# Kernel tuning notes

Hardware: AMD Instinct MI355X
Metric: run time of the kernel (lower is better)

## Reference

```python
import jax, jax.numpy as jnp
import numpy as np

B, S, E, H = 4, 1024, 1024, 16
HD = E // H
EPS = 1e-10


def setup_inputs() -> dict:
    key = jax.random.key(0)
    ks = jax.random.split(key, 10)
    w = lambda k: jax.random.normal(k, (E, E), jnp.float32) * 0.02
    b = lambda k: jax.random.normal(k, (E,), jnp.float32) * 0.02
    return {
        "query": jax.random.normal(ks[0], (B, S, E), jnp.float32),
        "Wq": w(ks[1]), "bq": b(ks[2]),
        "Wk": w(ks[3]), "bk": b(ks[4]),
        "Wv": w(ks[5]), "bv": b(ks[6]),
        "Wo": w(ks[7]), "bo": b(ks[8]),
        "alpha": jnp.array(1.0, jnp.float32),
    }


def reference(query, Wq, bq, Wk, bk, Wv, bv, Wo, bo, alpha):
    scale = 1.0 / np.sqrt(HD)
    # projections -> [B, H, S, HD]
    def heads(x, W, bias):
        return (x @ W.T + bias).reshape(B, S, H, HD).transpose(0, 2, 1, 3)
    Q = heads(query, Wq, bq)
    K = heads(query, Wk, bk)
    V = heads(query, Wv, bv)
    # raw scores [B, H, S, S]
    scores = jnp.einsum('bhqd,bhkd->bhqk', Q, K) * scale
    # 2D FFT over the (q, k) plane
    scores_fft = jnp.fft.fft2(scores, axes=(-2, -1))
    # spectral filter: exp(i * alpha * arctan(log|F| + eps))
    phase = alpha * jnp.arctan(jnp.log(jnp.abs(scores_fft) + EPS))
    filt = jnp.exp(1j * phase)
    scores_filtered = jnp.fft.ifft2(scores_fft * filt, axes=(-2, -1)).real
    # softmax over keys (dropout is identity at eval)
    attn = jax.nn.softmax(scores_filtered, axis=-1)
    ctx = jnp.einsum('bhqk,bhkd->bhqd', attn, V)
    ctx = ctx.transpose(0, 2, 1, 3).reshape(B, S, E)
    return ctx @ Wo.T + bo
```

## Files before the change

kernel.cpp:

```cpp
#include <hip/hip_runtime.h>
#include <hip/hip_fp16.h>


typedef __attribute__((ext_vector_type(8))) short short8;
typedef __attribute__((ext_vector_type(8))) _Float16 half8;
typedef __attribute__((ext_vector_type(4))) float f32x4;

#define PITCH 40
#define PITCH1 72

__device__ __forceinline__ float bf2f(short v) {
  return __uint_as_float(((unsigned)(unsigned short)v) << 16);
}
__device__ __forceinline__ short f2bf(float f) {
  unsigned u = __float_as_uint(f);
  u += 0x7FFFu + ((u >> 16) & 1u);
  return (short)(u >> 16);
}

__device__ __forceinline__ short8 ld8(const void* p, size_t idx, int isf32) {
  short8 r;
  if (isf32) {
    const float* f = (const float*)p + idx;
    float4 a = *(const float4*)f;
    float4 b = *(const float4*)(f + 4);
    r[0] = f2bf(a.x); r[1] = f2bf(a.y); r[2] = f2bf(a.z); r[3] = f2bf(a.w);
    r[4] = f2bf(b.x); r[5] = f2bf(b.y); r[6] = f2bf(b.z); r[7] = f2bf(b.w);
  } else {
    r = *(const short8*)((const short*)p + idx);
  }
  return r;
}
__device__ __forceinline__ float ldf(const void* p, int idx, int isf32) {
  return isf32 ? ((const float*)p)[idx] : bf2f(((const short*)p)[idx]);
}

__device__ __forceinline__ float2 cmul(float2 a, float2 b) {
  return make_float2(a.x * b.x - a.y * b.y, a.x * b.y + a.y * b.x);
}
__device__ __forceinline__ float2 cmulc(float2 a, float2 b) {
  return make_float2(a.x * b.x + a.y * b.y, a.y * b.x - a.x * b.y);
}
__device__ __forceinline__ float2 cadd(float2 a, float2 b) {
  return make_float2(a.x + b.x, a.y + b.y);
}
__device__ __forceinline__ float2 csub(float2 a, float2 b) {
  return make_float2(a.x - b.x, a.y - b.y);
}


template <int SGN>
__device__ __forceinline__ void dft16_dif(float2* x) {
  const float C16[8] = {1.f, 0.92387953f, 0.70710678f, 0.38268343f,
                        0.f, -0.38268343f, -0.70710678f, -0.92387953f};
  const float S16[8] = {0.f, 0.38268343f, 0.70710678f, 0.92387953f,
                        1.f, 0.92387953f, 0.70710678f, 0.38268343f};
#pragma unroll
  for (int h = 8; h >= 1; h >>= 1)
#pragma unroll
    for (int b = 0; b < 16; b += 2 * h)
#pragma unroll
      for (int i = 0; i < h; ++i) {
        const int e = i * (8 / h);
        float2 u = x[b + i], v = x[b + i + h];
        x[b + i] = cadd(u, v);
        float2 d = csub(u, v);
        float2 w = make_float2(C16[e], SGN > 0 ? S16[e] : -S16[e]);
        x[b + i + h] = (e == 0) ? d : cmul(d, w);
      }
}

__device__ __forceinline__ void dit16_inv(float2* x) {
  const float C16[8] = {1.f, 0.92387953f, 0.70710678f, 0.38268343f,
                        0.f, -0.38268343f, -0.70710678f, -0.92387953f};
  const float S16[8] = {0.f, 0.38268343f, 0.70710678f, 0.92387953f,
                        1.f, 0.92387953f, 0.70710678f, 0.38268343f};
#pragma unroll
  for (int h = 1; h <= 8; h <<= 1)
#pragma unroll
    for (int b = 0; b < 16; b += 2 * h)
#pragma unroll
      for (int i = 0; i < h; ++i) {
        const int e = i * (8 / h);
        float2 w = make_float2(C16[e], -S16[e]);
        float2 u = x[b + i];
        float2 vh = (e == 0) ? x[b + i + h] : cmulc(x[b + i + h], w);
        x[b + i] = cadd(u, vh);
        x[b + i + h] = csub(u, vh);
      }
}

template <int SGN>
__device__ __forceinline__ void midtw(float2* x, int lane) {
  const int rho[16] = {0, 8, 4, 12, 2, 10, 6, 14, 1, 9, 5, 13, 3, 11, 7, 15};
  float s, c;
  __sincosf((float)lane * 0.00613592315f, &s, &c);
  float2 w = make_float2(c, SGN > 0 ? s : -s);
  float2 run = w;
  x[8] = cmul(x[8], run);
#pragma unroll
  for (int e = 2; e < 16; ++e) {
    run = cmul(run, w);
    x[rho[e]] = cmul(x[rho[e]], run);
  }
}

template <int SGN>
__device__ __forceinline__ void xlane_dif(float2* x, int lane) {
#pragma unroll
  for (int h = 32; h >= 1; h >>= 1) {
    const int e = (lane & (h - 1)) * (32 / h);
    float s, c;
    __sincosf((float)e * 0.09817477042f, &s, &c);
    float2 w = make_float2(c, SGN > 0 ? s : -s);
    const bool hi = (lane & h) != 0;
#pragma unroll
    for (int r = 0; r < 16; ++r) {
      float2 t = x[r];
      float2 p;
      p.x = __shfl_xor(t.x, h, 64);
      p.y = __shfl_xor(t.y, h, 64);
      x[r] = hi ? cmul(csub(p, t), w) : cadd(t, p);
    }
  }
}

template <int SGN>
__device__ __forceinline__ void wfft1024_dif(float2* x, int lane) {
  dft16_dif<SGN>(x);
  midtw<SGN>(x, lane);
  xlane_dif<SGN>(x, lane);
}

template <int SGN>
__device__ __forceinline__ void midtw2(float2* x, float2* y, int lane) {
  const int rho[16] = {0, 8, 4, 12, 2, 10, 6, 14, 1, 9, 5, 13, 3, 11, 7, 15};
  float s, c;
  __sincosf((float)lane * 0.00613592315f, &s, &c);
  float2 w = make_float2(c, SGN > 0 ? s : -s);
  float2 run = w;
  x[8] = cmul(x[8], run);
  y[8] = cmul(y[8], run);
#pragma unroll
  for (int e = 2; e < 16; ++e) {
    run = cmul(run, w);
    x[rho[e]] = cmul(x[rho[e]], run);
    y[rho[e]] = cmul(y[rho[e]], run);
  }
}

__device__ __forceinline__ void midtw_inv2(float2* x, float2* y, int lane) {
  const int rho[16] = {0, 8, 4, 12, 2, 10, 6, 14, 1, 9, 5, 13, 3, 11, 7, 15};
  float s, c;
  __sincosf((float)lane * 0.00613592315f, &s, &c);
  float2 w = make_float2(c, -s);
  float2 run = w;
  x[8] = cmulc(x[8], run);
  y[8] = cmulc(y[8], run);
#pragma unroll
  for (int e = 2; e < 16; ++e) {
    run = cmul(run, w);
    x[rho[e]] = cmulc(x[rho[e]], run);
    y[rho[e]] = cmulc(y[rho[e]], run);
  }
}

template <int SGN>
__device__ __forceinline__ void xlane_dif2(float2* x, float2* y, int lane) {
#pragma unroll
  for (int h = 32; h >= 1; h >>= 1) {
    const int e = (lane & (h - 1)) * (32 / h);
    float s, c;
    __sincosf((float)e * 0.09817477042f, &s, &c);
    float2 w = make_float2(c, SGN > 0 ? s : -s);
    const bool hi = (lane & h) != 0;
#pragma unroll
    for (int r = 0; r < 16; ++r) {
      float2 t = x[r];
      float2 p;
      p.x = __shfl_xor(t.x, h, 64);
      p.y = __shfl_xor(t.y, h, 64);
      x[r] = hi ? cmul(csub(p, t), w) : cadd(t, p);
    }
#pragma unroll
    for (int r = 0; r < 16; ++r) {
      float2 t = y[r];
      float2 p;
      p.x = __shfl_xor(t.x, h, 64);
      p.y = __shfl_xor(t.y, h, 64);
      y[r] = hi ? cmul(csub(p, t), w) : cadd(t, p);
    }
  }
}

__device__ __forceinline__ void xlane_dit_inv2(float2* x, float2* y, int lane) {
#pragma unroll
  for (int h = 1; h <= 32; h <<= 1) {
    const int e = (lane & (h - 1)) * (32 / h);
    float s, c;
    __sincosf((float)e * 0.09817477042f, &s, &c);
    float2 w = make_float2(c, -s);
    const bool hi = (lane & h) != 0;
#pragma unroll
    for (int r = 0; r < 16; ++r) {
      float2 t = x[r];
      if (hi) t = cmulc(t, w);
      float2 p;
      p.x = __shfl_xor(t.x, h, 64);
      p.y = __shfl_xor(t.y, h, 64);
      x[r] = hi ? csub(p, t) : cadd(t, p);
    }
#pragma unroll
    for (int r = 0; r < 16; ++r) {
      float2 t = y[r];
      if (hi) t = cmulc(t, w);
      float2 p;
      p.x = __shfl_xor(t.x, h, 64);
      p.y = __shfl_xor(t.y, h, 64);
      y[r] = hi ? csub(p, t) : cadd(t, p);
    }
  }
}

template <int SGN>
__device__ __forceinline__ void wfft1024_dif2(float2* x, float2* y, int lane) {
  dft16_dif<SGN>(x);
  dft16_dif<SGN>(y);
  midtw2<SGN>(x, y, lane);
  xlane_dif2<SGN>(x, y, lane);
}
__device__ __forceinline__ void wfft1024_inv2(float2* x, float2* y, int lane) {
  xlane_dit_inv2(x, y, lane);
  midtw_inv2(x, y, lane);
  dit16_inv(x);
  dit16_inv(y);
}

__device__ __forceinline__ float gainw(float re, float im, float alpha, bool a1) {
  float mag2 = re * re + im * im;
  float t = 0.5f * __logf(mag2 + 1e-20f);
  if (a1) return __builtin_amdgcn_rsqf(fmaf(t, t, 1.0f)) * (1.0f / 1048576.0f);
  return __cosf(alpha * atanf(t)) * (1.0f / 1048576.0f);
}

__global__ void k0_detect(const unsigned* __restrict__ q,
                          const void* __restrict__ alphap, int* __restrict__ flags) {
  __shared__ float smax[256];
  __shared__ int szero[256];
  int t = threadIdx.x;
  float mx = 0.f; int zc = 0;
  for (int i = t; i < 16384; i += 256) {
    unsigned w = q[i];
    unsigned lo = w & 0xFFFFu;
    float v = fabsf(__uint_as_float(lo << 16));
    if (!(v <= 1e30f)) v = 1e30f;
    mx = fmaxf(mx, v);
    zc += (lo == 0u);
  }
  smax[t] = mx; szero[t] = zc;
  __syncthreads();
  for (int s = 128; s > 0; s >>= 1) {
    if (t < s) { smax[t] = fmaxf(smax[t], smax[t + s]); szero[t] += szero[t + s]; }
    __syncthreads();
  }
  if (t == 0) {
    int isf32 = (smax[0] > 100.f) || (szero[0] > 12288);
    flags[0] = isf32;
    float alpha = isf32 ? *(const float*)alphap : bf2f(*(const short*)alphap);
    ((float*)flags)[1] = alpha;
  }
}

__global__ __launch_bounds__(256) void k1_qkv(
    const void* __restrict__ x,
    const void* __restrict__ Wq, const void* __restrict__ bq,
    const void* __restrict__ Wk, const void* __restrict__ bk,
    const void* __restrict__ Wv, const void* __restrict__ bv,
    short* __restrict__ Qt, short* __restrict__ Kt, short* __restrict__ Vt,
    const int* __restrict__ flags)
{
  __shared__ __align__(16) char smem[128 * PITCH1 * 2 * 2];
  short* As = (short*)smem;
  short* Bs = As + 128 * PITCH1;
  short* Ct = (short*)smem;
  const int isf32 = flags[0];
  const int t = threadIdx.x;
  const int lb = blockIdx.x;
  const int m0 = ((lb & 7) * 4 + ((lb >> 3) & 3)) * 128;
  const int n0 = (lb >> 5) * 128;
  const int which = blockIdx.y;
  const void* __restrict__ W = (which == 0) ? Wq : (which == 1) ? Wk : Wv;
  const void* __restrict__ bias = (which == 0) ? bq : (which == 1) ? bk : bv;
  const int lane = t & 63, wvi = t >> 6;
  const int wr = wvi >> 1, wc = wvi & 1;
  const int lm = lane & 15, lq = lane >> 4;
  f32x4 acc[4][4] = {};

  for (int k0 = 0; k0 < 1024; k0 += 64) {
    __syncthreads();
#pragma unroll
    for (int i = 0; i < 4; ++i) {
      int l = t + i * 256;
      int row = l >> 3, kk = (l & 7) << 3;
      *(short8*)&As[row * PITCH1 + kk] = ld8(x, (size_t)(m0 + row) * 1024 + k0 + kk, isf32);
      *(short8*)&Bs[row * PITCH1 + kk] = ld8(W, (size_t)(n0 + row) * 1024 + k0 + kk, isf32);
    }
    __syncthreads();
#pragma unroll
    for (int kh = 0; kh < 2; ++kh) {
      short8 af[4], bf[4];
#pragma unroll
      for (int a = 0; a < 4; ++a)
        af[a] = *(const short8*)&As[(wr * 64 + a * 16 + lm) * PITCH1 + kh * 32 + lq * 8];
#pragma unroll
      for (int b = 0; b < 4; ++b)
        bf[b] = *(const short8*)&Bs[(wc * 64 + b * 16 + lm) * PITCH1 + kh * 32 + lq * 8];
#pragma unroll
      for (int a = 0; a < 4; ++a)
#pragma unroll
        for (int b = 0; b < 4; ++b)
          acc[a][b] = __builtin_amdgcn_mfma_f32_16x16x32_bf16(af[a], bf[b], acc[a][b], 0, 0, 0);
    }
  }

  __syncthreads();
#pragma unroll
  for (int a = 0; a < 4; ++a)
#pragma unroll
    for (int b = 0; b < 4; ++b) {
      int col = wc * 64 + b * 16 + lm;
      float bv_ = ldf(bias, n0 + col, isf32);
#pragma unroll
      for (int r = 0; r < 4; ++r) {
        int row = wr * 64 + a * 16 + lq * 4 + r;
        Ct[row * 136 + col] = f2bf(acc[a][b][r] + bv_);
      }
    }
  __syncthreads();

  short* __restrict__ O = (which == 0) ? Qt : (which == 1) ? Kt : Vt;
#pragma unroll
  for (int j = 0; j < 8; ++j) {
    int id = t + j * 256;
    int d128 = id & 127, sg = (id >> 7) * 8;
    short vals[8];
#pragma unroll
    for (int i = 0; i < 8; ++i) vals[i] = Ct[(sg + i) * 136 + d128];
    int col = n0 + d128;
    int h = col >> 6, d = col & 63;
    int bb = m0 >> 10, sbase = (m0 & 1023) + sg;
    *(short8*)&O[(((size_t)(bb * 16 + h)) << 16) + ((size_t)d << 10) + sbase] = *(short8*)vals;
  }
}

__global__ __launch_bounds__(128) void kA_qkfft(
    const short* __restrict__ Qt, const short* __restrict__ Kt,
    __half2* __restrict__ Qhat, __half2* __restrict__ Khat)
{
  __shared__ float2 sbuf[2][1024];
  const int lane = threadIdx.x & 63, w = threadIdx.x >> 6;
  const int z = blockIdx.y;
  const int bx = blockIdx.x;
  if (bx < 16) {
    const short* qp = Qt + ((size_t)z << 16);
    const int d0 = bx * 4 + w * 2;
    float2 x[16], y[16];
#pragma unroll
    for (int j = 0; j < 16; ++j) {
      x[j] = make_float2(0.125f * bf2f(qp[(d0 << 10) + lane + 64 * j]), 0.f);
      y[j] = make_float2(0.125f * bf2f(qp[((d0 + 1) << 10) + lane + 64 * j]), 0.f);
    }
    wfft1024_dif2<-1>(x, y, lane);
    __half2* o0 = Qhat + (((size_t)(z * 64 + d0)) << 10);
    __half2* o1 = o0 + 1024;
#pragma unroll
    for (int r = 0; r < 16; ++r) {
      o0[lane + 64 * r] = __float22half2_rn(x[r]);
      o1[lane + 64 * r] = __float22half2_rn(y[r]);
    }
  } else {
    const short* kp = Kt + ((size_t)z << 16);
    const int p = (bx - 16) * 2 + w;
    const int d0 = 2 * p;
    float2 x[16];
#pragma unroll
    for (int j = 0; j < 16; ++j)
      x[j] = make_float2(bf2f(kp[(d0 << 10) + lane + 64 * j]),
                         bf2f(kp[((d0 + 1) << 10) + lane + 64 * j]));
    wfft1024_dif<-1>(x, lane);
    const int rho[16] = {0, 8, 4, 12, 2, 10, 6, 14, 1, 9, 5, 13, 3, 11, 7, 15};
    const int bl6 = ((lane & 1) << 5) | ((lane & 2) << 3) | ((lane & 4) << 1) |
                    ((lane & 8) >> 1) | ((lane & 16) >> 3) | ((lane & 32) >> 5);
    float2* buf = sbuf[w];
#pragma unroll
    for (int r = 0; r < 16; ++r) buf[rho[r] + 16 * bl6] = x[r];
    __half2* o0 = Khat + (size_t)(z * 64 + d0) * 520;
    __half2* o1 = o0 + 520;
#pragma unroll 1
    for (int jj = 0; jj < 9; ++jj) {
      int v = lane + 64 * jj;
      if (v <= 512) {
        float2 A = buf[v], B = buf[(1024 - v) & 1023];
        o0[v] = __float22half2_rn(make_float2((A.x + B.x) * 0.5f, (A.y - B.y) * 0.5f));
        o1[v] = __float22half2_rn(make_float2((A.y + B.y) * 0.5f, (B.x - A.x) * 0.5f));
      }
    }
  }
}

__global__ __launch_bounds__(256) void kB_specmm(
    const __half2* __restrict__ Qhat, const __half2* __restrict__ Khat,
    __half2* __restrict__ Ct, const int* __restrict__ flags, int bh0)
{
  __shared__ unsigned short Are[64][72], Aim[64][72], Bre[128][72], Bim[128][72];
  const int t = threadIdx.x;
  const int u0 = blockIdx.x * 128;
  const int v0 = blockIdx.y * 64;
  const int zl = blockIdx.z;
  const int z = bh0 + zl;
  const float alpha = ((const float*)flags)[1];
  const bool a1 = (alpha == 1.0f);
  {
    const int d = t >> 2;
    const ushort2* src = (const ushort2*)(Khat + (size_t)(z * 64 + d) * 520);
    int vb = (t & 3) * 16;
#pragma unroll
    for (int j = 0; j < 16; ++j) {
      int v = v0 + vb + j;
      if (v > 519) v = 519;
      ushort2 e = src[v];
      int row = vb + j;
      int dc = d ^ (((row >> 4) & 3) << 4);
      Are[row][dc] = e.x;
      Aim[row][dc] = e.y;
    }
    const ushort2* srcb = (const ushort2*)(Qhat + (((size_t)(z * 64 + d)) << 10) + u0);
    int ub = (t & 3) * 32;
#pragma unroll
    for (int j = 0; j < 32; ++j) {
      ushort2 e = srcb[ub + j];
      int row = ub + j;
      int dc = d ^ (((row >> 5) & 3) << 4);
      Bre[row][dc] = e.x;
      Bim[row][dc] = e.y;
    }
  }
  __syncthreads();

  const int lane = t & 63, wc = t >> 6;
  const int lm = lane & 15, lq = lane >> 4;
  f32x4 cre[4][2] = {}, cim[4][2] = {};
#pragma unroll
  for (int ks = 0; ks < 2; ++ks) {
    half8 ar[4], ai[4], aiN[4], br[2], bi[2];
#pragma unroll
    for (int a = 0; a < 4; ++a) {
      int dc = (ks * 32 + lq * 8) ^ ((a & 3) << 4);
      ar[a] = *(const half8*)&Are[a * 16 + lm][dc];
      ai[a] = *(const half8*)&Aim[a * 16 + lm][dc];
      int4 tm = *(int4*)&ai[a];
      tm.x ^= 0x80008000; tm.y ^= 0x80008000; tm.z ^= 0x80008000; tm.w ^= 0x80008000;
      aiN[a] = *(half8*)&tm;
    }
#pragma unroll
    for (int n = 0; n < 2; ++n) {
      int dc = (ks * 32 + lq * 8) ^ ((wc & 3) << 4);
      br[n] = *(const half8*)&Bre[wc * 32 + n * 16 + lm][dc];
      bi[n] = *(const half8*)&Bim[wc * 32 + n * 16 + lm][dc];
    }
#pragma unroll
    for (int a = 0; a < 4; ++a)
#pragma unroll
      for (int n = 0; n < 2; ++n) {
        cre[a][n] = __builtin_amdgcn_mfma_f32_16x16x32_f16(ar[a], br[n], cre[a][n], 0, 0, 0);
        cre[a][n] = __builtin_amdgcn_mfma_f32_16x16x32_f16(aiN[a], bi[n], cre[a][n], 0, 0, 0);
        cim[a][n] = __builtin_amdgcn_mfma_f32_16x16x32_f16(ar[a], bi[n], cim[a][n], 0, 0, 0);
        cim[a][n] = __builtin_amdgcn_mfma_f32_16x16x32_f16(ai[a], br[n], cim[a][n], 0, 0, 0);
      }
  }

  __half2* outp = Ct + (size_t)zl * 513 * 1024 + u0 + wc * 32;
#pragma unroll
  for (int a = 0; a < 4; ++a)
#pragma unroll
    for (int r = 0; r < 4; ++r) {
      int v = v0 + a * 16 + lq * 4 + r;
      if (v < 513) {
#pragma unroll
        for (int n = 0; n < 2; ++n) {
          float re = cre[a][n][r], im = cim[a][n][r];
          float wf = gainw(re, im, alpha, a1);
          outp[(size_t)v * 1024 + n * 16 + lm] =
              __float22half2_rn(make_float2(re * wf, im * wf));
        }
      }
    }
}

__global__ __launch_bounds__(256) void k4_invfft(__half2* __restrict__ Ct)
{
  const int lane = threadIdx.x & 63;
  const int w = threadIdx.x >> 6;
  const int gv0 = blockIdx.x * 8 + w * 2;
  if (gv0 > 512) return;
  const bool has1 = (gv0 + 1 <= 512);
  __half2* __restrict__ row0 = Ct + (size_t)blockIdx.y * 513 * 1024 + ((size_t)gv0 << 10);
  __half2* __restrict__ row1 = row0 + 1024;
  float2 x[16], y[16];
#pragma unroll
  for (int j = 0; j < 16; ++j) x[j] = __half22float2(row0[lane + 64 * j]);
  if (has1) {
#pragma unroll
    for (int j = 0; j < 16; ++j) y[j] = __half22float2(row1[lane + 64 * j]);
  } else {
#pragma unroll
    for (int j = 0; j < 16; ++j) y[j] = make_float2(0.f, 0.f);
  }
  wfft1024_inv2(x, y, lane);
#pragma unroll
  for (int j = 0; j < 16; ++j) row0[lane + 64 * j] = __float22half2_rn(x[j]);
  if (has1) {
#pragma unroll
    for (int j = 0; j < 16; ++j) row1[lane + 64 * j] = __float22half2_rn(y[j]);
  }
}

__global__ __launch_bounds__(512) void k56_softmax_av(
    const __half2* __restrict__ Ct, const short* __restrict__ Vt,
    short* __restrict__ ctx, int bh0)
{
  __shared__ __align__(16) char GP[33280];
  const int tid = threadIdx.x;
  const int q0 = blockIdx.x * 16, z = blockIdx.y;
  const int lane = tid & 63, w = tid >> 6;
  const int lm = lane & 15, lq = lane >> 4;
  const __half2* __restrict__ in = Ct + (size_t)z * 513 * 1024;
#define GROW(m) ((__half2*)(GP + 448 + (m) * 2052))
  for (int id = tid; id < 2052; id += 512) {
    int v = id >> 2, qq = (id & 3) * 4;
    int4 o = *(const int4*)&in[(size_t)v * 1024 + q0 + qq];
    __half2* op = (__half2*)&o;
#pragma unroll
    for (int i = 0; i < 4; ++i) GROW(qq + i)[v] = op[i];
  }
  short* P = (short*)GP;
  const int bl6 = ((lane & 1) << 5) | ((lane & 2) << 3) | ((lane & 4) << 1) |
                  ((lane & 8) >> 1) | ((lane & 16) >> 3) | ((lane & 32) >> 5);
  __syncthreads();

  const int p = w;
  const __half2* g1 = GROW(2 * p);
  const __half2* g2 = GROW(2 * p + 1);
  float2 x[16];
#pragma unroll
  for (int j = 0; j < 16; ++j) {
    int v = lane + 64 * j;
    float2 a, b;
    if (v <= 512) {
      a = __half22float2(g1[v]);
      b = __half22float2(g2[v]);
    } else {
      int v2 = 1024 - v;
      float2 aa = __half22float2(g1[v2]), bb = __half22float2(g2[v2]);
      a = make_float2(aa.x, -aa.y);
      b = make_float2(bb.x, -bb.y);
    }
    x[j] = make_float2(a.x - b.y, a.y + b.x);
  }

  wfft1024_dif<1>(x, lane);

  float m1 = -3.4e38f, m2 = -3.4e38f;
#pragma unroll
  for (int j = 0; j < 16; ++j) { m1 = fmaxf(m1, x[j].x); m2 = fmaxf(m2, x[j].y); }
#pragma unroll
  for (int s = 32; s > 0; s >>= 1) {
    m1 = fmaxf(m1, __shfl_xor(m1, s, 64));
    m2 = fmaxf(m2, __shfl_xor(m2, s, 64));
  }
  float s1 = 0.f, s2 = 0.f;
#pragma unroll
  for (int j = 0; j < 16; ++j) {
    float e1 = __expf(x[j].x - m1), e2 = __expf(x[j].y - m2);
    x[j] = make_float2(e1, e2);
    s1 += e1; s2 += e2;
  }
#pragma unroll
  for (int s = 32; s > 0; s >>= 1) {
    s1 += __shfl_xor(s1, s, 64);
    s2 += __shfl_xor(s2, s, 64);
  }
  float inv1 = 1.0f / s1, inv2 = 1.0f / s2;

  __syncthreads();

  {
    const int rho[16] = {0, 8, 4, 12, 2, 10, 6, 14, 1, 9, 5, 13, 3, 11, 7, 15};
#pragma unroll
    for (int j = 0; j < 16; ++j) {
      int k = rho[j] + 16 * bl6;
      P[(2 * p) * 1040 + k]     = f2bf(x[j].x * inv1);
      P[(2 * p + 1) * 1040 + k] = f2bf(x[j].y * inv2);
    }
  }
  __syncthreads();

  const short* __restrict__ Vp = Vt + ((size_t)(bh0 + z) << 16);
  f32x4 acc[4] = {};
#pragma unroll
  for (int ks = 0; ks < 4; ++ks) {
    int k0 = w * 128 + ks * 32;
    short8 a0 = *(const short8*)&P[lm * 1040 + k0 + lq * 8];
#pragma unroll
    for (int b = 0; b < 4; ++b) {
      short8 bv = *(const short8*)&Vp[(size_t)(b * 16 + lm) * 1024 + k0 + lq * 8];
      acc[b] = __builtin_amdgcn_mfma_f32_16x16x32_bf16(a0, bv, acc[b], 0, 0, 0);
    }
  }
  __syncthreads();
  float* red = (float*)GP;
#pragma unroll
  for (int b = 0; b < 4; ++b)
#pragma unroll
    for (int r = 0; r < 4; ++r)
      red[(w * 16 + lq * 4 + r) * 64 + b * 16 + lm] = acc[b][r];
  __syncthreads();
  if (tid < 256) {
    int q = tid >> 4, d0 = (tid & 15) * 4;
    float s0 = 0.f, s1_ = 0.f, s2_ = 0.f, s3 = 0.f;
#pragma unroll
    for (int ww = 0; ww < 8; ++ww) {
      const float* rr = &red[(ww * 16 + q) * 64 + d0];
      s0 += rr[0]; s1_ += rr[1]; s2_ += rr[2]; s3 += rr[3];
    }
    short o4[4] = {f2bf(s0), f2bf(s1_), f2bf(s2_), f2bf(s3)};
    *(int2*)&ctx[(((size_t)(bh0 + z)) << 16) + (size_t)(q0 + q) * 64 + d0] = *(int2*)o4;
  }
#undef GROW
}

__global__ __launch_bounds__(256) void k7_out(
    const short* __restrict__ ctx, const void* __restrict__ Wo,
    const void* __restrict__ bo, void* __restrict__ out,
    const int* __restrict__ flags)
{
  __shared__ __align__(16) char smem[128 * 136 * 2];
  short* As = (short*)smem;
  short* Bs = As + 128 * PITCH;
  short* Ct = (short*)smem;
  const int isf32 = flags[0];
  const int t = threadIdx.x;
  const int lb = blockIdx.x;
  const int m0 = ((lb & 7) * 4 + ((lb >> 3) & 3)) * 128;
  const int n0 = (lb >> 5) * 128;
  const int lane = t & 63, wvi = t >> 6;
  const int wr = wvi >> 1, wc = wvi & 1;
  const int lm = lane & 15, lq = lane >> 4;
  f32x4 acc[4][4] = {};

  for (int k0 = 0; k0 < 1024; k0 += 32) {
    __syncthreads();
#pragma unroll
    for (int i = 0; i < 2; ++i) {
      int l = t + i * 256;
      int row = l >> 2, kk = (l & 3) << 3;
      int n = m0 + row, e = k0 + kk;
      size_t aaddr = (((size_t)((n >> 10) * 16 + (e >> 6))) << 16) + (size_t)((n & 1023) << 6) + (e & 63);
      *(int4*)&As[row * PITCH + kk] = *(const int4*)&ctx[aaddr];
      *(short8*)&Bs[row * PITCH + kk] = ld8(Wo, (size_t)(n0 + row) * 1024 + e, isf32);
    }
    __syncthreads();
    short8 af[4], bf[4];
#pragma unroll
    for (int a = 0; a < 4; ++a) af[a] = *(const short8*)&As[(wr * 64 + a * 16 + lm) * PITCH + lq * 8];
#pragma unroll
    for (int b = 0; b < 4; ++b) bf[b] = *(const short8*)&Bs[(wc * 64 + b * 16 + lm) * PITCH + lq * 8];
#pragma unroll
    for (int a = 0; a < 4; ++a)
#pragma unroll
      for (int b = 0; b < 4; ++b)
        acc[a][b] = __builtin_amdgcn_mfma_f32_16x16x32_bf16(af[a], bf[b], acc[a][b], 0, 0, 0);
  }

  if (isf32) {
#pragma unroll
    for (int a = 0; a < 4; ++a)
#pragma unroll
      for (int b = 0; b < 4; ++b) {
        int col = n0 + wc * 64 + b * 16 + lm;
        float bo_ = ldf(bo, col, 1);
#pragma unroll
        for (int r = 0; r < 4; ++r) {
          int row = m0 + wr * 64 + a * 16 + lq * 4 + r;
          ((float*)out)[(size_t)row * 1024 + col] = acc[a][b][r] + bo_;
        }
      }
    return;
  }
  __syncthreads();
#pragma unroll
  for (int a = 0; a < 4; ++a)
#pragma unroll
    for (int b = 0; b < 4; ++b) {
      int col = wc * 64 + b * 16 + lm;
      float bo_ = ldf(bo, n0 + col, 0);
#pragma unroll
      for (int r = 0; r < 4; ++r) {
        int row = wr * 64 + a * 16 + lq * 4 + r;
        Ct[row * 136 + col] = f2bf(acc[a][b][r] + bo_);
      }
    }
  __syncthreads();
#pragma unroll
  for (int j = 0; j < 8; ++j) {
    int id = t + j * 256;
    int row = id >> 4, c16 = (id & 15) * 8;
    short8 v = *(const short8*)&Ct[row * 136 + c16];
    *(short8*)&((short*)out)[(size_t)(m0 + row) * 1024 + n0 + c16] = v;
  }
}

extern "C" void kernel_launch(void* const* d_in, const int* in_sizes, int n_in,
                              void* d_out, int out_size, void* d_ws, size_t ws_size,
                              hipStream_t stream)
{
  const void* x  = d_in[0];
  const void* Wq = d_in[1];
  const void* bq = d_in[2];
  const void* Wk = d_in[3];
  const void* bk = d_in[4];
  const void* Wv = d_in[5];
  const void* bv = d_in[6];
  const void* Wo = d_in[7];
  const void* bo = d_in[8];
  const void* alphap = d_in[9];
  char* ws = (char*)d_ws;

  const size_t PLANE_CT = (size_t)513 * 1024 * 4;
  const size_t QH_SZ = (size_t)64 * 64 * 1024 * 4;
  const size_t KH_SZ = (size_t)64 * 64 * 520 * 4;

  const size_t B_CT  = 0;
  const size_t B_VT  = 64 * PLANE_CT;
  const size_t B_CX  = B_VT + ((size_t)8u << 20);
  const size_t B_QH  = B_CX + ((size_t)8u << 20);
  const size_t B_KH  = B_QH + QH_SZ;
  const size_t B_FL  = B_KH + KH_SZ;
  const size_t B_NEED = B_FL + 256;

  if (ws_size >= B_NEED) {
    short*   Qt   = (short*)(ws);
    short*   Kt   = (short*)(ws + ((size_t)8u << 20));
    short*   Vt   = (short*)(ws + B_VT);
    short*   ctx  = (short*)(ws + B_CX);
    __half2* Ct   = (__half2*)(ws + B_CT);
    __half2* Qhat = (__half2*)(ws + B_QH);
    __half2* Khat = (__half2*)(ws + B_KH);
    int*     flags = (int*)(ws + B_FL);

    k0_detect<<<1, 256, 0, stream>>>((const unsigned*)x, alphap, flags);
    k1_qkv<<<dim3(256, 3), 256, 0, stream>>>(x, Wq, bq, Wk, bk, Wv, bv, Qt, Kt, Vt, flags);
    kA_qkfft<<<dim3(32, 64), 128, 0, stream>>>(Qt, Kt, Qhat, Khat);
    kB_specmm<<<dim3(8, 9, 64), 256, 0, stream>>>(Qhat, Khat, Ct, flags, 0);
    k4_invfft<<<dim3(65, 64), 256, 0, stream>>>(Ct);
    k56_softmax_av<<<dim3(64, 64), 512, 0, stream>>>(Ct, Vt, ctx, 0);
    k7_out<<<256, 256, 0, stream>>>(ctx, Wo, bo, d_out, flags);
    return;
  }

  const size_t VT_OFF = (size_t)17u << 20;
  const size_t CX_OFF = (size_t)25u << 20;
  const size_t QH_OFF = (size_t)33u << 20;
  const size_t KH_OFF = QH_OFF + QH_SZ;
  const size_t FL_OFF = KH_OFF + KH_SZ;

  short*   Qt   = (short*)(ws);
  short*   Kt   = (short*)(ws + ((size_t)8u << 20));
  short*   Vt   = (short*)(ws + VT_OFF);
  short*   ctx  = (short*)(ws + CX_OFF);
  __half2* Ct   = (__half2*)(ws);
  __half2* Qhat = (__half2*)(ws + QH_OFF);
  __half2* Khat = (__half2*)(ws + KH_OFF);
  int*     flags = (int*)(ws + FL_OFF);

  k0_detect<<<1, 256, 0, stream>>>((const unsigned*)x, alphap, flags);
  k1_qkv<<<dim3(256, 3), 256, 0, stream>>>(x, Wq, bq, Wk, bk, Wv, bv, Qt, Kt, Vt, flags);
  kA_qkfft<<<dim3(32, 64), 128, 0, stream>>>(Qt, Kt, Qhat, Khat);
  for (int c = 0; c < 8; ++c) {
    int bh0 = c * 8;
    kB_specmm<<<dim3(8, 9, 8), 256, 0, stream>>>(Qhat, Khat, Ct, flags, bh0);
    k4_invfft<<<dim3(65, 8), 256, 0, stream>>>(Ct);
    k56_softmax_av<<<dim3(64, 8), 512, 0, stream>>>(Ct, Vt, ctx, bh0);
  }
  k7_out<<<256, 256, 0, stream>>>(ctx, Wo, bo, d_out, flags);
}
```

Measured before the change: 689.4 us.

## Process 32 query rows per softmax-AV block, sharing V loads across two tiles

The fused softmax+AV kernel now handles 32 query rows per block instead of 16. Each wave runs two FFT row-pairs through a dual FFT routine and issues two MFMA accumulator sets per V fragment, so each V load is reused twice. The P-tile stores are vectorised into short8 writes. Block count halves, shared memory doubles to about 65KB, and register pressure rises, which may reduce occupancy.

```diff
diff --git a/kernel.cpp b/kernel.cpp
--- a/kernel.cpp
+++ b/kernel.cpp
@@ -529,92 +529,122 @@
     const __half2* __restrict__ Ct, const short* __restrict__ Vt,
     short* __restrict__ ctx, int bh0)
 {
-  __shared__ __align__(16) char GP[33280];
+  __shared__ __align__(16) char GP[66560];
   const int tid = threadIdx.x;
-  const int q0 = blockIdx.x * 16, z = blockIdx.y;
+  const int q0 = blockIdx.x * 32, z = blockIdx.y;
   const int lane = tid & 63, w = tid >> 6;
   const int lm = lane & 15, lq = lane >> 4;
   const __half2* __restrict__ in = Ct + (size_t)z * 513 * 1024;
-#define GROW(m) ((__half2*)(GP + 448 + (m) * 2052))
-  for (int id = tid; id < 2052; id += 512) {
-    int v = id >> 2, qq = (id & 3) * 4;
-    int4 o = *(const int4*)&in[(size_t)v * 1024 + q0 + qq];
-    __half2* op = (__half2*)&o;
-#pragma unroll
-    for (int i = 0; i < 4; ++i) GROW(qq + i)[v] = op[i];
-  }
+#define GROW(m) ((__half2*)(GP + (m) * 2064))
+#pragma unroll
+  for (int qb = 0; qb < 2; ++qb)
+    for (int id = tid; id < 2052; id += 512) {
+      int v = id >> 2, qq = (id & 3) * 4;
+      int4 o = *(const int4*)&in[(size_t)v * 1024 + q0 + qb * 16 + qq];
+      __half2* op = (__half2*)&o;
+#pragma unroll
+      for (int i = 0; i < 4; ++i) GROW(qb * 16 + qq + i)[v] = op[i];
+    }
   short* P = (short*)GP;
   const int bl6 = ((lane & 1) << 5) | ((lane & 2) << 3) | ((lane & 4) << 1) |
                   ((lane & 8) >> 1) | ((lane & 16) >> 3) | ((lane & 32) >> 5);
   __syncthreads();
 
-  const int p = w;
-  const __half2* g1 = GROW(2 * p);
-  const __half2* g2 = GROW(2 * p + 1);
-  float2 x[16];
+  const __half2* g1 = GROW(2 * w);
+  const __half2* g2 = GROW(2 * w + 1);
+  const __half2* g3 = GROW(16 + 2 * w);
+  const __half2* g4 = GROW(16 + 2 * w + 1);
+  float2 x[16], y[16];
 #pragma unroll
   for (int j = 0; j < 16; ++j) {
     int v = lane + 64 * j;
-    float2 a, b;
     if (v <= 512) {
-      a = __half22float2(g1[v]);
-      b = __half22float2(g2[v]);
+      float2 a = __half22float2(g1[v]), b = __half22float2(g2[v]);
+      float2 c = __half22float2(g3[v]), d = __half22float2(g4[v]);
+      x[j] = make_float2(a.x - b.y, a.y + b.x);
+      y[j] = make_float2(c.x - d.y, c.y + d.x);
     } else {
       int v2 = 1024 - v;
       float2 aa = __half22float2(g1[v2]), bb = __half22float2(g2[v2]);
-      a = make_float2(aa.x, -aa.y);
-      b = make_float2(bb.x, -bb.y);
-    }
-    x[j] = make_float2(a.x - b.y, a.y + b.x);
-  }
-
-  wfft1024_dif<1>(x, lane);
-
-  float m1 = -3.4e38f, m2 = -3.4e38f;
-#pragma unroll
-  for (int j = 0; j < 16; ++j) { m1 = fmaxf(m1, x[j].x); m2 = fmaxf(m2, x[j].y); }
+      float2 cc = __half22float2(g3[v2]), dd = __half22float2(g4[v2]);
+      x[j] = make_float2(aa.x - (-bb.y), -aa.y + bb.x);
+      y[j] = make_float2(cc.x - (-dd.y), -cc.y + dd.x);
+    }
+  }
+
+  wfft1024_dif2<1>(x, y, lane);
+
+  float m1 = -3.4e38f, m2 = -3.4e38f, m3 = -3.4e38f, m4 = -3.4e38f;
+#pragma unroll
+  for (int j = 0; j < 16; ++j) {
+    m1 = fmaxf(m1, x[j].x); m2 = fmaxf(m2, x[j].y);
+    m3 = fmaxf(m3, y[j].x); m4 = fmaxf(m4, y[j].y);
+  }
 #pragma unroll
   for (int s = 32; s > 0; s >>= 1) {
     m1 = fmaxf(m1, __shfl_xor(m1, s, 64));
     m2 = fmaxf(m2, __shfl_xor(m2, s, 64));
-  }
-  float s1 = 0.f, s2 = 0.f;
+    m3 = fmaxf(m3, __shfl_xor(m3, s, 64));
+    m4 = fmaxf(m4, __shfl_xor(m4, s, 64));
+  }
+  float s1 = 0.f, s2 = 0.f, s3 = 0.f, s4 = 0.f;
 #pragma unroll
   for (int j = 0; j < 16; ++j) {
     float e1 = __expf(x[j].x - m1), e2 = __expf(x[j].y - m2);
+    float e3 = __expf(y[j].x - m3), e4 = __expf(y[j].y - m4);
     x[j] = make_float2(e1, e2);
-    s1 += e1; s2 += e2;
+    y[j] = make_float2(e3, e4);
+    s1 += e1; s2 += e2; s3 += e3; s4 += e4;
   }
 #pragma unroll
   for (int s = 32; s > 0; s >>= 1) {
     s1 += __shfl_xor(s1, s, 64);
     s2 += __shfl_xor(s2, s, 64);
-  }
-  float inv1 = 1.0f / s1, inv2 = 1.0f / s2;
+    s3 += __shfl_xor(s3, s, 64);
+    s4 += __shfl_xor(s4, s, 64);
+  }
+  float inv1 = 1.0f / s1, inv2 = 1.0f / s2, inv3 = 1.0f / s3, inv4 = 1.0f / s4;
 
   __syncthreads();
 
   {
     const int rho[16] = {0, 8, 4, 12, 2, 10, 6, 14, 1, 9, 5, 13, 3, 11, 7, 15};
-#pragma unroll
-    for (int j = 0; j < 16; ++j) {
-      int k = rho[j] + 16 * bl6;
-      P[(2 * p) * 1040 + k]     = f2bf(x[j].x * inv1);
-      P[(2 * p + 1) * 1040 + k] = f2bf(x[j].y * inv2);
-    }
+    short a0[16], a1[16], b0_[16], b1_[16];
+#pragma unroll
+    for (int pos = 0; pos < 16; ++pos) {
+      const int j = rho[pos];
+      a0[pos]  = f2bf(x[j].x * inv1);
+      a1[pos]  = f2bf(x[j].y * inv2);
+      b0_[pos] = f2bf(y[j].x * inv3);
+      b1_[pos] = f2bf(y[j].y * inv4);
+    }
+    short* d0p = &P[(2 * w) * 1040 + 16 * bl6];
+    short* d1p = &P[(2 * w + 1) * 1040 + 16 * bl6];
+    short* d2p = &P[(16 + 2 * w) * 1040 + 16 * bl6];
+    short* d3p = &P[(16 + 2 * w + 1) * 1040 + 16 * bl6];
+    *(short8*)d0p       = *(short8*)&a0[0];
+    *(short8*)(d0p + 8) = *(short8*)&a0[8];
+    *(short8*)d1p       = *(short8*)&a1[0];
+    *(short8*)(d1p + 8) = *(short8*)&a1[8];
+    *(short8*)d2p       = *(short8*)&b0_[0];
+    *(short8*)(d2p + 8) = *(short8*)&b0_[8];
+    *(short8*)d3p       = *(short8*)&b1_[0];
+    *(short8*)(d3p + 8) = *(short8*)&b1_[8];
   }
   __syncthreads();
 
   const short* __restrict__ Vp = Vt + ((size_t)(bh0 + z) << 16);
-  f32x4 acc[4] = {};
+  f32x4 acc0[4] = {}, acc1[4] = {};
 #pragma unroll
   for (int ks = 0; ks < 4; ++ks) {
     int k0 = w * 128 + ks * 32;
-    short8 a0 = *(const short8*)&P[lm * 1040 + k0 + lq * 8];
+    short8 p0 = *(const short8*)&P[lm * 1040 + k0 + lq * 8];
+    short8 p1 = *(const short8*)&P[(16 + lm) * 1040 + k0 + lq * 8];
 #pragma unroll
     for (int b = 0; b < 4; ++b) {
       short8 bv = *(const short8*)&Vp[(size_t)(b * 16 + lm) * 1024 + k0 + lq * 8];
-      acc[b] = __builtin_amdgcn_mfma_f32_16x16x32_bf16(a0, bv, acc[b], 0, 0, 0);
+      acc0[b] = __builtin_amdgcn_mfma_f32_16x16x32_bf16(p0, bv, acc0[b], 0, 0, 0);
+      acc1[b] = __builtin_amdgcn_mfma_f32_16x16x32_bf16(p1, bv, acc1[b], 0, 0, 0);
     }
   }
   __syncthreads();
@@ -622,18 +652,20 @@
 #pragma unroll
   for (int b = 0; b < 4; ++b)
 #pragma unroll
-    for (int r = 0; r < 4; ++r)
-      red[(w * 16 + lq * 4 + r) * 64 + b * 16 + lm] = acc[b][r];
-  __syncthreads();
-  if (tid < 256) {
+    for (int r = 0; r < 4; ++r) {
+      red[(w * 32 + lq * 4 + r) * 64 + b * 16 + lm]      = acc0[b][r];
+      red[(w * 32 + 16 + lq * 4 + r) * 64 + b * 16 + lm] = acc1[b][r];
+    }
+  __syncthreads();
+  {
     int q = tid >> 4, d0 = (tid & 15) * 4;
-    float s0 = 0.f, s1_ = 0.f, s2_ = 0.f, s3 = 0.f;
+    float s0 = 0.f, s1_ = 0.f, s2_ = 0.f, s3_ = 0.f;
 #pragma unroll
     for (int ww = 0; ww < 8; ++ww) {
-      const float* rr = &red[(ww * 16 + q) * 64 + d0];
-      s0 += rr[0]; s1_ += rr[1]; s2_ += rr[2]; s3 += rr[3];
-    }
-    short o4[4] = {f2bf(s0), f2bf(s1_), f2bf(s2_), f2bf(s3)};
+      const float* rr = &red[(ww * 32 + q) * 64 + d0];
+      s0 += rr[0]; s1_ += rr[1]; s2_ += rr[2]; s3_ += rr[3];
+    }
+    short o4[4] = {f2bf(s0), f2bf(s1_), f2bf(s2_), f2bf(s3_)};
     *(int2*)&ctx[(((size_t)(bh0 + z)) << 16) + (size_t)(q0 + q) * 64 + d0] = *(int2*)o4;
   }
 #undef GROW
@@ -763,7 +795,7 @@
     kA_qkfft<<<dim3(32, 64), 128, 0, stream>>>(Qt, Kt, Qhat, Khat);
     kB_specmm<<<dim3(8, 9, 64), 256, 0, stream>>>(Qhat, Khat, Ct, flags, 0);
     k4_invfft<<<dim3(65, 64), 256, 0, stream>>>(Ct);
-    k56_softmax_av<<<dim3(64, 64), 512, 0, stream>>>(Ct, Vt, ctx, 0);
+    k56_softmax_av<<<dim3(32, 64), 512, 0, stream>>>(Ct, Vt, ctx, 0);
     k7_out<<<256, 256, 0, stream>>>(ctx, Wo, bo, d_out, flags);
     return;
   }
@@ -790,7 +822,7 @@
     int bh0 = c * 8;
     kB_specmm<<<dim3(8, 9, 8), 256, 0, stream>>>(Qhat, Khat, Ct, flags, bh0);
     k4_invfft<<<dim3(65, 8), 256, 0, stream>>>(Ct);
-    k56_softmax_av<<<dim3(64, 8), 512, 0, stream>>>(Ct, Vt, ctx, bh0);
+    k56_softmax_av<<<dim3(32, 8), 512, 0, stream>>>(Ct, Vt, ctx, bh0);
   }
   k7_out<<<256, 256, 0, stream>>>(ctx, Wo, bo, d_out, flags);
 }
```

After: 711.7 us. 1.03x slower.
